# Kernel tuning notes

Hardware: AMD Instinct MI355X
Metric: run time of the kernel (lower is better)

## Reference

```python
import jax, jax.numpy as jnp
import numpy as np

MARGIN = 1.0
EPS = 1e-7  # added to the difference vector, matching F.pairwise_distance


def setup_inputs() -> dict:
    key = jax.random.key(0)
    k1, k2, k3 = jax.random.split(key, 3)
    B, D = 8192, 512
    feats = jax.random.normal(k1, (B, D), dtype=jnp.float32)
    labels = jax.random.randint(k2, (B,), 0, 2).astype(jnp.int64)
    # noise[0] drives positive sampling, noise[1] drives negative sampling
    noise = jax.random.uniform(k3, (2, B, B), dtype=jnp.float32)
    return {"feats": feats, "labels": labels, "noise": noise}


def reference(feats, labels, noise):
    # feats: [B, D], labels: [B] in {0,1}, noise: [2, B, B]
    pos_mask = labels[None, :] == labels[:, None]        # [B, B] same-label
    neg_mask = labels[None, :] == (1 - labels)[:, None]  # [B, B] opposite-label

    # Uniform sample among matching indices via argmax of masked iid uniforms.
    pos_idx = jnp.argmax(jnp.where(pos_mask, noise[0], -1.0), axis=1)  # [B]
    neg_idx = jnp.argmax(jnp.where(neg_mask, noise[1], -1.0), axis=1)  # [B]

    # Positive set always contains the anchor itself (count >= 1).
    positive = feats[pos_idx]                                           # [B, D]
    # If no negatives exist, the original falls back to the anchor feat.
    has_neg = neg_mask.any(axis=1)                                      # [B]
    negative = jnp.where(has_neg[:, None], feats[neg_idx], feats)       # [B, D]

    # TripletMarginLoss(margin=1, p=2, eps=1e-7), reduction='mean'
    d_ap = jnp.linalg.norm(feats - positive + EPS, axis=1)
    d_an = jnp.linalg.norm(feats - negative + EPS, axis=1)
    return jnp.mean(jax.nn.relu(d_ap - d_an + MARGIN))
```

## Files before the change

kernel.cpp:

```cpp
#include <hip/hip_runtime.h>

constexpr int Bn = 8192;
constexpr int Dn = 512;
constexpr int ROWS_PER_BLOCK = 4;
#define EPSF 1e-7f
#define MARGINF 1.0f

__device__ __forceinline__ void amax_combine(float& bv, int& bi, float v, int i) {
    if (v > bv || (v == bv && i < bi)) { bv = v; bi = i; }
}

__global__ __launch_bounds__(256) void scan_kernel(
    const int*   __restrict__ labels,
    const float* __restrict__ noise,
    int2*        __restrict__ idx_out)
{
    __shared__ unsigned slab_u[Bn / 4];
    __shared__ int s_any;
    __shared__ float swv[ROWS_PER_BLOCK * 8];
    __shared__ int   swi[ROWS_PER_BLOCK * 8];

    const int tid  = threadIdx.x;
    const int lane = tid & 63;
    const int wv   = tid >> 6;

    if (tid == 0) s_any = 0;
    __syncthreads();
    if (tid < 128 && labels[2 * tid + 1] != 0) atomicOr(&s_any, 1);
    __syncthreads();
    const bool is64 = (s_any == 0);

    if (is64) {
        const long long* l8 = (const long long*)labels;
        for (int w = tid; w < Bn / 4; w += 256) {
            unsigned b0 = (unsigned)l8[w * 4 + 0] & 0xffu;
            unsigned b1 = (unsigned)l8[w * 4 + 1] & 0xffu;
            unsigned b2 = (unsigned)l8[w * 4 + 2] & 0xffu;
            unsigned b3 = (unsigned)l8[w * 4 + 3] & 0xffu;
            slab_u[w] = b0 | (b1 << 8) | (b2 << 16) | (b3 << 24);
        }
    } else {
        for (int w = tid; w < Bn / 4; w += 256) {
            int4 v = ((const int4*)labels)[w];
            slab_u[w] = ((unsigned)v.x & 0xffu) | (((unsigned)v.y & 0xffu) << 8) |
                        (((unsigned)v.z & 0xffu) << 16) | (((unsigned)v.w & 0xffu) << 24);
        }
    }
    __syncthreads();

    char* slab = (char*)slab_u;

    for (int r = 0; r < ROWS_PER_BLOCK; ++r) {
        const int row = blockIdx.x * ROWS_PER_BLOCK + r;
        const char myLab = slab[row];

        const float* __restrict__ n0 = noise + (size_t)row * Bn;
        const float* __restrict__ n1 = noise + (size_t)Bn * Bn + (size_t)row * Bn;

        float pbv[4] = {-1.0f, -1.0f, -1.0f, -1.0f};
        float nbv[4] = {-1.0f, -1.0f, -1.0f, -1.0f};
        int   pbi[4] = {0x7FFFFFFF, 0x7FFFFFFF, 0x7FFFFFFF, 0x7FFFFFFF};
        int   nbi[4] = {0x7FFFFFFF, 0x7FFFFFFF, 0x7FFFFFFF, 0x7FFFFFFF};

#pragma unroll 2
        for (int j = tid * 4; j < Bn; j += 256 * 4) {
            float4 v0 = *(const float4*)(n0 + j);
            float4 v1 = *(const float4*)(n1 + j);
            unsigned lw = slab_u[j >> 2];
            const float* f0 = (const float*)&v0;
            const float* f1 = (const float*)&v1;
#pragma unroll
            for (int k = 0; k < 4; ++k) {
                char lk = (char)((lw >> (k * 8)) & 0xffu);
                float cp = (lk == myLab) ? f0[k] : -1.0f;
                if (cp > pbv[k]) { pbv[k] = cp; pbi[k] = j + k; }
                float cn = (lk != myLab) ? f1[k] : -1.0f;
                if (cn > nbv[k]) { nbv[k] = cn; nbi[k] = j + k; }
            }
        }

        float pv = pbv[0]; int pi_ = pbi[0];
        float nv = nbv[0]; int ni_ = nbi[0];
#pragma unroll
        for (int k = 1; k < 4; ++k) {
            amax_combine(pv, pi_, pbv[k], pbi[k]);
            amax_combine(nv, ni_, nbv[k], nbi[k]);
        }

        for (int off = 32; off; off >>= 1) {
            float ov = __shfl_down(pv, off, 64);
            int   oi = __shfl_down(pi_, off, 64);
            amax_combine(pv, pi_, ov, oi);
            ov = __shfl_down(nv, off, 64);
            oi = __shfl_down(ni_, off, 64);
            amax_combine(nv, ni_, ov, oi);
        }
        const int r8 = r * 8;
        if (lane == 0) { swv[r8 + wv] = pv; swi[r8 + wv] = pi_;
                         swv[r8 + 4 + wv] = nv; swi[r8 + 4 + wv] = ni_; }
        __syncthreads();

        if (tid == 0) {
            float bv = swv[r8]; int bi = swi[r8];
#pragma unroll
            for (int k = 1; k < 4; ++k) amax_combine(bv, bi, swv[r8 + k], swi[r8 + k]);
            float bv2 = swv[r8 + 4]; int bi2 = swi[r8 + 4];
#pragma unroll
            for (int k = 5; k < 8; ++k) amax_combine(bv2, bi2, swv[r8 + k], swi[r8 + k]);
            idx_out[row] = make_int2(bi, (bv2 >= 0.0f) ? bi2 : row);
        }
    }
}

__global__ __launch_bounds__(256) void dist_kernel(
    const float* __restrict__ feats,
    const int2*  __restrict__ idx,
    float*       __restrict__ losses)
{
    const int tid  = threadIdx.x;
    const int lane = tid & 63;
    const int wv   = tid >> 6;
    const int row  = blockIdx.x * 4 + wv;

    const int2 pn = idx[row];
    const float* fa = feats + (size_t)row  * Dn;
    const float* fp = feats + (size_t)pn.x * Dn;
    const float* fn = feats + (size_t)pn.y * Dn;

    float dap = 0.0f, dan = 0.0f;
#pragma unroll
    for (int c = 0; c < 2; ++c) {
        const int o = c * 256 + lane * 4;
        float4 a = *(const float4*)(fa + o);
        float4 p = *(const float4*)(fp + o);
        float4 q = *(const float4*)(fn + o);
        float d;
        d = a.x - p.x + EPSF; dap += d * d;
        d = a.y - p.y + EPSF; dap += d * d;
        d = a.z - p.z + EPSF; dap += d * d;
        d = a.w - p.w + EPSF; dap += d * d;
        d = a.x - q.x + EPSF; dan += d * d;
        d = a.y - q.y + EPSF; dan += d * d;
        d = a.z - q.z + EPSF; dan += d * d;
        d = a.w - q.w + EPSF; dan += d * d;
    }
    for (int off = 32; off; off >>= 1) {
        dap += __shfl_down(dap, off, 64);
        dan += __shfl_down(dan, off, 64);
    }
    if (lane == 0)
        losses[row] = fmaxf(sqrtf(dap) - sqrtf(dan) + MARGINF, 0.0f);
}

__global__ __launch_bounds__(256) void reduce_mean_kernel(
    const float* __restrict__ losses, float* __restrict__ out)
{
    const int tid  = threadIdx.x;
    const int lane = tid & 63;
    const int wv   = tid >> 6;
    float s = 0.0f;
    for (int k = tid; k < Bn; k += 256) s += losses[k];
    for (int off = 32; off; off >>= 1) s += __shfl_down(s, off, 64);
    __shared__ float sw[4];
    if (lane == 0) sw[wv] = s;
    __syncthreads();
    if (tid == 0) out[0] = (sw[0] + sw[1] + sw[2] + sw[3]) * (1.0f / (float)Bn);
}

extern "C" void kernel_launch(void* const* d_in, const int* in_sizes, int n_in,
                              void* d_out, int out_size, void* d_ws, size_t ws_size,
                              hipStream_t stream) {
    const float* feats  = (const float*)d_in[0];
    const int*   labels = (const int*)d_in[1];
    const float* noise  = (const float*)d_in[2];

    int2*  idx    = (int2*)d_ws;
    float* losses = (float*)((char*)d_ws + 65536);

    scan_kernel<<<Bn / ROWS_PER_BLOCK, 256, 0, stream>>>(labels, noise, idx);
    dist_kernel<<<Bn / 4, 256, 0, stream>>>(feats, idx, losses);
    reduce_mean_kernel<<<1, 256, 0, stream>>>(losses, (float*)d_out);
}
```

Baseline: 124.6 us.

## Pack labels into bitmask once and scan one noise row per block

A new one-block kernel packs the labels into a 1-bit-per-sample mask, so each scan block no longer reloads and repacks all 8192 labels. The scan kernel now launches one block per (row, pos/neg) pair, giving 16384 small blocks with each thread reading 8 consecutive floats. Blocks no longer need several barriers per row, and the per-block label preprocessing that competed with the 512 MB noise stream is gone. It adds an extra kernel launch and more block-scheduling overhead.

After: 122.5 us. Within noise of the previous version (-1.7%).

```diff
diff --git a/kernel.cpp b/kernel.cpp
--- a/kernel.cpp
+++ b/kernel.cpp
@@ -2,7 +2,6 @@
 
 constexpr int Bn = 8192;
 constexpr int Dn = 512;
-constexpr int ROWS_PER_BLOCK = 4;
 #define EPSF 1e-7f
 #define MARGINF 1.0f
 
@@ -10,111 +9,100 @@
     if (v > bv || (v == bv && i < bi)) { bv = v; bi = i; }
 }
 
+__global__ __launch_bounds__(256) void pack_labels_kernel(const int* __restrict__ labels,
+                                                          unsigned* __restrict__ bits) {
+    const int tid  = threadIdx.x;
+    const int lane = tid & 63;
+    const int wv   = tid >> 6;
+    __shared__ int s_any;
+    if (tid == 0) s_any = 0;
+    __syncthreads();
+    if (tid < 128 && labels[2 * tid + 1] != 0) atomicOr(&s_any, 1);
+    __syncthreads();
+    const bool is64 = (s_any == 0);
+    const long long* l8 = (const long long*)labels;
+    for (int r = 0; r < 32; ++r) {
+        const int idx = r * 256 + tid;
+        unsigned v = is64 ? (unsigned)l8[idx] : (unsigned)labels[idx];
+        unsigned long long m = __ballot(v & 1u);
+        if (lane == 0) {
+            const int w0 = (r * 256 + wv * 64) >> 5;
+            bits[w0]     = (unsigned)m;
+            bits[w0 + 1] = (unsigned)(m >> 32);
+        }
+    }
+}
+
 __global__ __launch_bounds__(256) void scan_kernel(
-    const int*   __restrict__ labels,
-    const float* __restrict__ noise,
-    int2*        __restrict__ idx_out)
+    const unsigned* __restrict__ bits,
+    const float*    __restrict__ noise,
+    int*            __restrict__ pos_idx,
+    int*            __restrict__ neg_idx)
 {
-    __shared__ unsigned slab_u[Bn / 4];
-    __shared__ int s_any;
-    __shared__ float swv[ROWS_PER_BLOCK * 8];
-    __shared__ int   swi[ROWS_PER_BLOCK * 8];
+    __shared__ unsigned sbits[Bn / 32];
+    __shared__ float swv[4];
+    __shared__ int   swi[4];
 
     const int tid  = threadIdx.x;
     const int lane = tid & 63;
     const int wv   = tid >> 6;
 
-    if (tid == 0) s_any = 0;
+    sbits[tid] = bits[tid];
     __syncthreads();
-    if (tid < 128 && labels[2 * tid + 1] != 0) atomicOr(&s_any, 1);
-    __syncthreads();
-    const bool is64 = (s_any == 0);
 
-    if (is64) {
-        const long long* l8 = (const long long*)labels;
-        for (int w = tid; w < Bn / 4; w += 256) {
-            unsigned b0 = (unsigned)l8[w * 4 + 0] & 0xffu;
-            unsigned b1 = (unsigned)l8[w * 4 + 1] & 0xffu;
-            unsigned b2 = (unsigned)l8[w * 4 + 2] & 0xffu;
-            unsigned b3 = (unsigned)l8[w * 4 + 3] & 0xffu;
-            slab_u[w] = b0 | (b1 << 8) | (b2 << 16) | (b3 << 24);
-        }
-    } else {
-        for (int w = tid; w < Bn / 4; w += 256) {
-            int4 v = ((const int4*)labels)[w];
-            slab_u[w] = ((unsigned)v.x & 0xffu) | (((unsigned)v.y & 0xffu) << 8) |
-                        (((unsigned)v.z & 0xffu) << 16) | (((unsigned)v.w & 0xffu) << 24);
+    const bool neg = (blockIdx.x >= Bn);
+    const int  row = neg ? (blockIdx.x - Bn) : blockIdx.x;
+
+    const unsigned myb = (sbits[row >> 5] >> (row & 31)) & 1u;
+    const unsigned xm  = myb ? 0xFFFFFFFFu : 0u;
+
+    const float* __restrict__ src = noise + (neg ? (size_t)Bn * Bn : (size_t)0)
+                                          + (size_t)row * Bn;
+
+    float bv[8] = {-1,-1,-1,-1,-1,-1,-1,-1};
+    int   bi[8] = {0x7FFFFFFF,0x7FFFFFFF,0x7FFFFFFF,0x7FFFFFFF,
+                   0x7FFFFFFF,0x7FFFFFFF,0x7FFFFFFF,0x7FFFFFFF};
+
+#pragma unroll
+    for (int it = 0; it < 4; ++it) {
+        const int j = tid * 8 + it * 2048;
+        float4 va = *(const float4*)(src + j);
+        float4 vb = *(const float4*)(src + j + 4);
+        unsigned u = (sbits[(tid >> 2) + it * 64] >> ((tid & 3) * 8)) ^ xm;
+        if (!neg) u = ~u;
+        const float f[8] = {va.x, va.y, va.z, va.w, vb.x, vb.y, vb.z, vb.w};
+#pragma unroll
+        for (int k = 0; k < 8; ++k) {
+            float c = ((u >> k) & 1u) ? f[k] : -1.0f;
+            if (c > bv[k]) { bv[k] = c; bi[k] = j + k; }
         }
     }
+
+    float v = bv[0]; int i = bi[0];
+#pragma unroll
+    for (int k = 1; k < 8; ++k) amax_combine(v, i, bv[k], bi[k]);
+
+    for (int off = 32; off; off >>= 1) {
+        float ov = __shfl_down(v, off, 64);
+        int   oi = __shfl_down(i, off, 64);
+        amax_combine(v, i, ov, oi);
+    }
+    if (lane == 0) { swv[wv] = v; swi[wv] = i; }
     __syncthreads();
 
-    char* slab = (char*)slab_u;
-
-    for (int r = 0; r < ROWS_PER_BLOCK; ++r) {
-        const int row = blockIdx.x * ROWS_PER_BLOCK + r;
-        const char myLab = slab[row];
-
-        const float* __restrict__ n0 = noise + (size_t)row * Bn;
-        const float* __restrict__ n1 = noise + (size_t)Bn * Bn + (size_t)row * Bn;
-
-        float pbv[4] = {-1.0f, -1.0f, -1.0f, -1.0f};
-        float nbv[4] = {-1.0f, -1.0f, -1.0f, -1.0f};
-        int   pbi[4] = {0x7FFFFFFF, 0x7FFFFFFF, 0x7FFFFFFF, 0x7FFFFFFF};
-        int   nbi[4] = {0x7FFFFFFF, 0x7FFFFFFF, 0x7FFFFFFF, 0x7FFFFFFF};
-
-#pragma unroll 2
-        for (int j = tid * 4; j < Bn; j += 256 * 4) {
-            float4 v0 = *(const float4*)(n0 + j);
-            float4 v1 = *(const float4*)(n1 + j);
-            unsigned lw = slab_u[j >> 2];
-            const float* f0 = (const float*)&v0;
-            const float* f1 = (const float*)&v1;
+    if (tid == 0) {
+        float fv = swv[0]; int fi = swi[0];
 #pragma unroll
-            for (int k = 0; k < 4; ++k) {
-                char lk = (char)((lw >> (k * 8)) & 0xffu);
-                float cp = (lk == myLab) ? f0[k] : -1.0f;
-                if (cp > pbv[k]) { pbv[k] = cp; pbi[k] = j + k; }
-                float cn = (lk != myLab) ? f1[k] : -1.0f;
-                if (cn > nbv[k]) { nbv[k] = cn; nbi[k] = j + k; }
-            }
-        }
-
-        float pv = pbv[0]; int pi_ = pbi[0];
-        float nv = nbv[0]; int ni_ = nbi[0];
-#pragma unroll
-        for (int k = 1; k < 4; ++k) {
-            amax_combine(pv, pi_, pbv[k], pbi[k]);
-            amax_combine(nv, ni_, nbv[k], nbi[k]);
-        }
-
-        for (int off = 32; off; off >>= 1) {
-            float ov = __shfl_down(pv, off, 64);
-            int   oi = __shfl_down(pi_, off, 64);
-            amax_combine(pv, pi_, ov, oi);
-            ov = __shfl_down(nv, off, 64);
-            oi = __shfl_down(ni_, off, 64);
-            amax_combine(nv, ni_, ov, oi);
-        }
-        const int r8 = r * 8;
-        if (lane == 0) { swv[r8 + wv] = pv; swi[r8 + wv] = pi_;
-                         swv[r8 + 4 + wv] = nv; swi[r8 + 4 + wv] = ni_; }
-        __syncthreads();
-
-        if (tid == 0) {
-            float bv = swv[r8]; int bi = swi[r8];
-#pragma unroll
-            for (int k = 1; k < 4; ++k) amax_combine(bv, bi, swv[r8 + k], swi[r8 + k]);
-            float bv2 = swv[r8 + 4]; int bi2 = swi[r8 + 4];
-#pragma unroll
-            for (int k = 5; k < 8; ++k) amax_combine(bv2, bi2, swv[r8 + k], swi[r8 + k]);
-            idx_out[row] = make_int2(bi, (bv2 >= 0.0f) ? bi2 : row);
-        }
+        for (int k = 1; k < 4; ++k) amax_combine(fv, fi, swv[k], swi[k]);
+        if (neg) neg_idx[row] = (fv >= 0.0f) ? fi : row;
+        else     pos_idx[row] = fi;
     }
 }
 
 __global__ __launch_bounds__(256) void dist_kernel(
     const float* __restrict__ feats,
-    const int2*  __restrict__ idx,
+    const int*   __restrict__ pos_idx,
+    const int*   __restrict__ neg_idx,
     float*       __restrict__ losses)
 {
     const int tid  = threadIdx.x;
@@ -122,10 +110,11 @@
     const int wv   = tid >> 6;
     const int row  = blockIdx.x * 4 + wv;
 
-    const int2 pn = idx[row];
-    const float* fa = feats + (size_t)row  * Dn;
-    const float* fp = feats + (size_t)pn.x * Dn;
-    const float* fn = feats + (size_t)pn.y * Dn;
+    const int pi = pos_idx[row];
+    const int ni = neg_idx[row];
+    const float* fa = feats + (size_t)row * Dn;
+    const float* fp = feats + (size_t)pi  * Dn;
+    const float* fn = feats + (size_t)ni  * Dn;
 
     float dap = 0.0f, dan = 0.0f;
 #pragma unroll
@@ -174,10 +163,13 @@
     const int*   labels = (const int*)d_in[1];
     const float* noise  = (const float*)d_in[2];
 
-    int2*  idx    = (int2*)d_ws;
-    float* losses = (float*)((char*)d_ws + 65536);
+    int*      pos_idx = (int*)d_ws;
+    int*      neg_idx = (int*)((char*)d_ws + 32768);
+    float*    losses  = (float*)((char*)d_ws + 65536);
+    unsigned* bits    = (unsigned*)((char*)d_ws + 98304);
 
-    scan_kernel<<<Bn / ROWS_PER_BLOCK, 256, 0, stream>>>(labels, noise, idx);
-    dist_kernel<<<Bn / 4, 256, 0, stream>>>(feats, idx, losses);
+    pack_labels_kernel<<<1, 256, 0, stream>>>(labels, bits);
+    scan_kernel<<<2 * Bn, 256, 0, stream>>>(bits, noise, pos_idx, neg_idx);
+    dist_kernel<<<Bn / 4, 256, 0, stream>>>(feats, pos_idx, neg_idx, losses);
     reduce_mean_kernel<<<1, 256, 0, stream>>>(losses, (float*)d_out);
 }
```
